# Kernel tuning notes

Hardware: AMD Instinct MI355X
Metric: run time of the kernel (lower is better)

## Reference

```python
import jax, jax.numpy as jnp
import numpy as np
from jax import lax

H = 1028  # hidden_size


def _lstm_layer(x, w_ih, w_hh, b_ih, b_hh):
    # x: [B, T, in], w_ih: [4H, in], w_hh: [4H, H] (PyTorch gate order i,f,g,o)
    B, T, _ = x.shape
    h_dim = w_hh.shape[1]
    # Precompute input contribution for all timesteps (memory-bound GEMM)
    xg = jnp.einsum('bti,gi->btg', x, w_ih) + b_ih + b_hh  # [B, T, 4H]

    def step(carry, xt):
        h, c = carry
        g = xt + h @ w_hh.T  # [B, 4H]
        i, f, gg, o = jnp.split(g, 4, axis=-1)
        i = jax.nn.sigmoid(i)
        f = jax.nn.sigmoid(f)
        gg = jnp.tanh(gg)
        o = jax.nn.sigmoid(o)
        c = f * c + i * gg
        h = o * jnp.tanh(c)
        return (h, c), h

    h0 = jnp.zeros((B, h_dim), x.dtype)
    c0 = jnp.zeros((B, h_dim), x.dtype)
    _, hs = lax.scan(step, (h0, c0), jnp.swapaxes(xg, 0, 1))  # [T, B, H]
    return jnp.swapaxes(hs, 0, 1)  # [B, T, H]


def setup_inputs() -> dict:
    key = jax.random.key(0)
    ks = jax.random.split(key, 12)
    s = 1.0 / np.sqrt(H)  # torch LSTM/Linear init scale

    def u(k, shape):
        return jax.random.uniform(k, shape, jnp.float32, -s, s)

    x = jax.random.normal(ks[0], (1, 16384, 1), dtype=jnp.float32)
    return {
        'x': x,
        'w_ih0': u(ks[1], (4 * H, 1)),
        'w_hh0': u(ks[2], (4 * H, H)),
        'b_ih0': u(ks[3], (4 * H,)),
        'b_hh0': u(ks[4], (4 * H,)),
        'w_ih1': u(ks[5], (4 * H, H)),
        'w_hh1': u(ks[6], (4 * H, H)),
        'b_ih1': u(ks[7], (4 * H,)),
        'b_hh1': u(ks[8], (4 * H,)),
        'lin_w': u(ks[9], (1, H)),
        'lin_b': u(ks[10], (1,)),
    }


def reference(x, w_ih0, w_hh0, b_ih0, b_hh0, w_ih1, w_hh1, b_ih1, b_hh1, lin_w, lin_b):
    h1 = _lstm_layer(x, w_ih0, w_hh0, b_ih0, b_hh0)   # [B, T, H]
    h2 = _lstm_layer(h1, w_ih1, w_hh1, b_ih1, b_hh1)  # [B, T, H]
    return h2 @ lin_w.T + lin_b                        # [B, T, 1]
```

## Files before the change

### kernel.cpp

```cpp
#include <hip/hip_runtime.h>
#include <math.h>

#define HH    1028
#define TT    16384
#define UP    1056
#define HSU   1056
#define HS    1056
#define NWG0  66
#define NWG1  132
#define NWGT  (NWG0 + NWG1)
#define R0    1024
#define R0M   (R0 - 1)
#define R1M   15

typedef unsigned long long u64;

__device__ __forceinline__ u64 ld_u64(const u64* p) {
    return __hip_atomic_load(p, __ATOMIC_RELAXED, __HIP_MEMORY_SCOPE_AGENT);
}
__device__ __forceinline__ void st_u64(u64* p, u64 v) {
    __hip_atomic_store(p, v, __ATOMIC_RELAXED, __HIP_MEMORY_SCOPE_AGENT);
}
__device__ __forceinline__ unsigned ld_u32(const unsigned* p) {
    return __hip_atomic_load(p, __ATOMIC_RELAXED, __HIP_MEMORY_SCOPE_AGENT);
}
__device__ __forceinline__ void st_u32(unsigned* p, unsigned v) {
    __hip_atomic_store(p, v, __ATOMIC_RELAXED, __HIP_MEMORY_SCOPE_AGENT);
}
__device__ __forceinline__ float sigmf(float x) { return 1.0f / (1.0f + expf(-x)); }
__device__ __forceinline__ u64 pack(unsigned tag, float v) {
    return ((u64)tag << 32) | (u64)__float_as_uint(v);
}

__device__ __forceinline__ void stage132(const u64* __restrict__ src, float* __restrict__ lds,
                                         int base, int lane, unsigned want, long long& budget) {
    const int i0 = base + lane, i1 = base + 64 + lane, i2 = base + 128 + lane;
    bool d0 = false, d1 = false, d2 = (lane >= 4);
    int spin = 2;
    for (;;) {
        if (!d0) { u64 v = ld_u64(src + i0);
                   if ((unsigned)(v >> 32) == want) { lds[i0] = __uint_as_float((unsigned)v); d0 = true; } }
        if (!d1) { u64 v = ld_u64(src + i1);
                   if ((unsigned)(v >> 32) == want) { lds[i1] = __uint_as_float((unsigned)v); d1 = true; } }
        if (!d2) { u64 v = ld_u64(src + i2);
                   if ((unsigned)(v >> 32) == want) { lds[i2] = __uint_as_float((unsigned)v); d2 = true; } }
        if (__all(d0 & d1 & d2)) break;
        if (--budget < 0) break;
        if (spin > 0) { --spin; continue; }
        __builtin_amdgcn_s_sleep(1);
    }
}

__device__ __forceinline__ void stage264(const u64* __restrict__ src, float* __restrict__ lds,
                                         int base, int lane, unsigned want, long long& budget) {
    const int i0 = base + lane, i1 = i0 + 64, i2 = i0 + 128, i3 = i0 + 192, i4 = i0 + 256;
    bool d0 = false, d1 = false, d2 = false, d3 = false, d4 = (lane >= 8);
    int spin = 2;
    for (;;) {
        if (!d0) { u64 v = ld_u64(src + i0);
                   if ((unsigned)(v >> 32) == want) { lds[i0] = __uint_as_float((unsigned)v); d0 = true; } }
        if (!d1) { u64 v = ld_u64(src + i1);
                   if ((unsigned)(v >> 32) == want) { lds[i1] = __uint_as_float((unsigned)v); d1 = true; } }
        if (!d2) { u64 v = ld_u64(src + i2);
                   if ((unsigned)(v >> 32) == want) { lds[i2] = __uint_as_float((unsigned)v); d2 = true; } }
        if (!d3) { u64 v = ld_u64(src + i3);
                   if ((unsigned)(v >> 32) == want) { lds[i3] = __uint_as_float((unsigned)v); d3 = true; } }
        if (!d4) { u64 v = ld_u64(src + i4);
                   if ((unsigned)(v >> 32) == want) { lds[i4] = __uint_as_float((unsigned)v); d4 = true; } }
        if (__all(d0 & d1 & d2 & d3 & d4)) break;
        if (--budget < 0) break;
        if (spin > 0) { --spin; continue; }
        __builtin_amdgcn_s_sleep(1);
    }
}

__global__ __launch_bounds__(1024, 4) void wn_fused(
    const float* __restrict__ x,
    const float* __restrict__ w_ih0, const float* __restrict__ w_hh0,
    const float* __restrict__ b_ih0, const float* __restrict__ b_hh0,
    const float* __restrict__ w_ih1, const float* __restrict__ w_hh1,
    const float* __restrict__ b_ih1, const float* __restrict__ b_hh1,
    u64* __restrict__ ring0,
    u64* __restrict__ ring1,
    float* __restrict__ h2hist,
    unsigned* __restrict__ l1prog)
{
    __shared__ float smem[4 * UP + 128];
    const int tid  = threadIdx.x;
    const int lane = tid & 63;
    const int w    = tid >> 6;

    for (int i = tid; i < 4 * UP + 128; i += 1024) smem[i] = 0.0f;

    if (blockIdx.x < NWG0) {
        float* hbuf = smem;
        float* gbuf = smem + 2 * UP;
        const int wg   = blockIdx.x;
        const int row  = tid >> 4;
        const int k0   = tid & 15;
        const int gate = row >> 4;
        const int du   = row & 15;
        const int u    = wg * 16 + du;
        const bool real = (u < HH);
        const int wr   = gate * HH + (real ? u : 0);

        float wv[16][4], wt0 = 0.f, wt1 = 0.f;
#pragma unroll
        for (int m = 0; m < 16; ++m) {
            const int j = k0 * 4 + m * 64;
#pragma unroll
            for (int q = 0; q < 4; ++q)
                wv[m][q] = (real && j + q < HH) ? w_hh0[(size_t)wr * HH + j + q] : 0.0f;
        }
        {   const int j = 1024 + k0 * 2;
            wt0 = (real && j     < HH) ? w_hh0[(size_t)wr * HH + j]     : 0.0f;
            wt1 = (real && j + 1 < HH) ? w_hh0[(size_t)wr * HH + j + 1] : 0.0f; }
#pragma unroll
        for (int m = 0; m < 16; ++m)
#pragma unroll
            for (int q = 0; q < 4; ++q) asm volatile("" : "+v"(wv[m][q]));
        asm volatile("" : "+v"(wt0), "+v"(wt1));

        const float wx = real ? w_ih0[wr] : 0.0f;
        const float bs = real ? (b_ih0[wr] + b_hh0[wr]) : 0.0f;
        __syncthreads();

        long long budget = 20000000LL;
        float c_reg = 0.0f;
        for (int t = 0; t < TT; ++t) {
            if (t > 0) {
                if (w == 0) {
                    const float* gl = gbuf + ((t - 1) & 1) * 64;
                    if (lane < 16) {
                        const float gi = gl[lane], gf = gl[16 + lane];
                        const float gg = gl[32 + lane], go = gl[48 + lane];
                        const float iv = sigmf(gi), fv = sigmf(gf), gv = tanhf(gg), ov = sigmf(go);
                        c_reg = fv * c_reg + iv * gv;
                        float hv = ov * tanhf(c_reg);
                        if (wg * 16 + lane >= HH) hv = 0.0f;
                        st_u64(ring0 + (size_t)((t - 1) & R0M) * HSU + wg * 16 + lane,
                               pack((unsigned)t, hv));
                    }
                } else if (w >= 4 && w < 12) {
                    stage132(ring0 + (size_t)((t - 1) & R0M) * HSU, hbuf + (t & 1) * UP,
                             (w - 4) * 132, lane, (unsigned)t, budget);
                } else if (w == 1 && lane == 0 && (t & 255) == 0) {
                    for (;;) {
                        unsigned p = ld_u32(l1prog);
                        if ((int)t - (int)p < R0 - 256) break;
                        if (--budget < 0) break;
                        __builtin_amdgcn_s_sleep(32);
                    }
                }
            }
            __syncthreads();
            const float* hb = hbuf + (t & 1) * UP;
            float acc = 0.0f;
#pragma unroll
            for (int m = 0; m < 16; ++m) {
                const float4 hv = *(const float4*)&hb[k0 * 4 + m * 64];
                acc = fmaf(wv[m][0], hv.x, acc);
                acc = fmaf(wv[m][1], hv.y, acc);
                acc = fmaf(wv[m][2], hv.z, acc);
                acc = fmaf(wv[m][3], hv.w, acc);
            }
            {   const float2 hv = *(const float2*)&hb[1024 + k0 * 2];
                acc = fmaf(wt0, hv.x, acc);
                acc = fmaf(wt1, hv.y, acc); }
#pragma unroll
            for (int off = 1; off < 16; off <<= 1) acc += __shfl_xor(acc, off);
            if (k0 == 0) gbuf[(t & 1) * 64 + row] = acc + x[t] * wx + bs;
            __syncthreads();
        }
        if (w == 0 && lane < 16) {
            const float* gl = gbuf + ((TT - 1) & 1) * 64;
            const float gi = gl[lane], gf = gl[16 + lane];
            const float gg = gl[32 + lane], go = gl[48 + lane];
            const float iv = sigmf(gi), fv = sigmf(gf), gv = tanhf(gg), ov = sigmf(go);
            c_reg = fv * c_reg + iv * gv;
            float hv = ov * tanhf(c_reg);
            if (wg * 16 + lane >= HH) hv = 0.0f;
            st_u64(ring0 + (size_t)((TT - 1) & R0M) * HSU + wg * 16 + lane,
                   pack((unsigned)TT, hv));
        }
    } else {
        float* abuf = smem;
        float* bbuf = smem + 2 * UP;
        float* gbuf = smem + 4 * UP;
        const int wg   = blockIdx.x - NWG0;
        const int row  = tid >> 5;
        const int k0   = tid & 31;
        const int gate = row >> 3;
        const int du   = row & 7;
        const int u    = wg * 8 + du;
        const bool real = (u < HH);
        const int wr   = gate * HH + (real ? u : 0);

        float wiv[8][4], whv[8][4], wit = 0.f, wht = 0.f;
#pragma unroll
        for (int m = 0; m < 8; ++m) {
            const int j = k0 * 4 + m * 128;
#pragma unroll
            for (int q = 0; q < 4; ++q) {
                const bool inb = real && (j + q < HH);
                wiv[m][q] = inb ? w_ih1[(size_t)wr * HH + j + q] : 0.0f;
                whv[m][q] = inb ? w_hh1[(size_t)wr * HH + j + q] : 0.0f;
            }
        }
        {   const int j = 1024 + k0;
            wit = (real && j < HH) ? w_ih1[(size_t)wr * HH + j] : 0.0f;
            wht = (real && j < HH) ? w_hh1[(size_t)wr * HH + j] : 0.0f; }
#pragma unroll
        for (int m = 0; m < 8; ++m)
#pragma unroll
            for (int q = 0; q < 4; ++q) {
                asm volatile("" : "+v"(wiv[m][q]));
                asm volatile("" : "+v"(whv[m][q]));
            }
        asm volatile("" : "+v"(wit), "+v"(wht));
        const float bs = real ? (b_ih1[wr] + b_hh1[wr]) : 0.0f;
        __syncthreads();

        long long budget = 20000000LL;
        float c_reg = 0.0f;
        for (int t = 0; t < TT; ++t) {
            if (w == 0) {
                if (t > 0) {
                    const float* gl = gbuf + ((t - 1) & 1) * 32;
                    if (lane < 8) {
                        const float gi = gl[lane], gf = gl[8 + lane];
                        const float gg = gl[16 + lane], go = gl[24 + lane];
                        const float iv = sigmf(gi), fv = sigmf(gf), gv = tanhf(gg), ov = sigmf(go);
                        c_reg = fv * c_reg + iv * gv;
                        float hv = ov * tanhf(c_reg);
                        if (wg * 8 + lane >= HH) hv = 0.0f;
                        st_u64(ring1 + (size_t)((t - 1) & R1M) * HSU + wg * 8 + lane,
                               pack((unsigned)t, hv));
                        h2hist[(size_t)(t - 1) * HS + wg * 8 + lane] = hv;
                    }
                }
            } else if (w >= 4 && w < 12) {
                if (t > 0)
                    stage132(ring1 + (size_t)((t - 1) & R1M) * HSU, bbuf + (t & 1) * UP,
                             (w - 4) * 132, lane, (unsigned)t, budget);
            } else if (w >= 12) {
                stage264(ring0 + (size_t)(t & R0M) * HSU, abuf + (t & 1) * UP,
                         (w - 12) * 264, lane, (unsigned)(t + 1), budget);
            }
            __syncthreads();
            const float* ab = abuf + (t & 1) * UP;
            const float* bb = bbuf + (t & 1) * UP;
            float acc = 0.0f;
#pragma unroll
            for (int m = 0; m < 8; ++m) {
                const float4 ha = *(const float4*)&ab[k0 * 4 + m * 128];
                const float4 hb2 = *(const float4*)&bb[k0 * 4 + m * 128];
                acc = fmaf(wiv[m][0], ha.x, acc);
                acc = fmaf(wiv[m][1], ha.y, acc);
                acc = fmaf(wiv[m][2], ha.z, acc);
                acc = fmaf(wiv[m][3], ha.w, acc);
                acc = fmaf(whv[m][0], hb2.x, acc);
                acc = fmaf(whv[m][1], hb2.y, acc);
                acc = fmaf(whv[m][2], hb2.z, acc);
                acc = fmaf(whv[m][3], hb2.w, acc);
            }
            acc = fmaf(wit, ab[1024 + k0], acc);
            acc = fmaf(wht, bb[1024 + k0], acc);
#pragma unroll
            for (int off = 1; off < 32; off <<= 1) acc += __shfl_xor(acc, off);
            if (k0 == 0) gbuf[(t & 1) * 32 + row] = acc + bs;
            __syncthreads();
            if (w == 1 && lane == 0 && wg == 0 && (t & 255) == 255)
                st_u32(l1prog, (unsigned)(t + 1));
        }
        if (w == 0 && lane < 8) {
            const float* gl = gbuf + ((TT - 1) & 1) * 32;
            const float gi = gl[lane], gf = gl[8 + lane];
            const float gg = gl[16 + lane], go = gl[24 + lane];
            const float iv = sigmf(gi), fv = sigmf(gf), gv = tanhf(gg), ov = sigmf(go);
            c_reg = fv * c_reg + iv * gv;
            float hv = ov * tanhf(c_reg);
            if (wg * 8 + lane >= HH) hv = 0.0f;
            h2hist[(size_t)(TT - 1) * HS + wg * 8 + lane] = hv;
        }
    }
}

__global__ __launch_bounds__(256) void wn_proj(
    const float* __restrict__ h2,
    const float* __restrict__ lin_w,
    const float* __restrict__ lin_b,
    float* __restrict__ out)
{
    const int lane = threadIdx.x & 63;
    const int wv   = threadIdx.x >> 6;
    const int t    = blockIdx.x * 4 + wv;
    const float* hp = h2 + (size_t)t * HS;
    float acc = 0.0f;
#pragma unroll
    for (int m = 0; m < 4; ++m) {
        const int j = lane * 4 + m * 256;
        const float4 h4 = *(const float4*)(hp + j);
        const float4 w4 = *(const float4*)(lin_w + j);
        acc += h4.x * w4.x + h4.y * w4.y + h4.z * w4.z + h4.w * w4.w;
    }
    if (lane == 0) {
#pragma unroll
        for (int j = 1024; j < HH; ++j) acc += hp[j] * lin_w[j];
    }
#pragma unroll
    for (int off = 1; off < 64; off <<= 1) acc += __shfl_xor(acc, off);
    if (lane == 0) out[t] = acc + lin_b[0];
}

extern "C" void kernel_launch(void* const* d_in, const int* in_sizes, int n_in,
                              void* d_out, int out_size, void* d_ws, size_t ws_size,
                              hipStream_t stream) {
    const float* x     = (const float*)d_in[0];
    const float* w_ih0 = (const float*)d_in[1];
    const float* w_hh0 = (const float*)d_in[2];
    const float* b_ih0 = (const float*)d_in[3];
    const float* b_hh0 = (const float*)d_in[4];
    const float* w_ih1 = (const float*)d_in[5];
    const float* w_hh1 = (const float*)d_in[6];
    const float* b_ih1 = (const float*)d_in[7];
    const float* b_hh1 = (const float*)d_in[8];
    const float* lin_w = (const float*)d_in[9];
    const float* lin_b = (const float*)d_in[10];
    float* out = (float*)d_out;

    char* ws = (char*)d_ws;
    const size_t R0B = (size_t)R0 * HSU * 8;
    const size_t R1B = (size_t)16 * HSU * 8;
    const size_t H2B = (size_t)TT * HS * 4;
    u64* ring0 = (u64*)(ws);
    u64* ring1 = (u64*)(ws + R0B);
    float* h2hist = (float*)(ws + R0B + R1B);
    unsigned* l1prog = (unsigned*)(ws + R0B + R1B + H2B);

    wn_fused<<<NWGT, 1024, 0, stream>>>(x, w_ih0, w_hh0, b_ih0, b_hh0,
                                        w_ih1, w_hh1, b_ih1, b_hh1,
                                        ring0, ring1, h2hist, l1prog);
    wn_proj<<<TT / 4, 256, 0, stream>>>(h2hist, lin_w, lin_b, out);
}
```

Baseline: 43.81 ms.

## Remap waves so each owns one hidden unit and drop the second barrier per step

Work is reassigned so each wavefront computes all four gate dot products for one hidden unit (layer 0) or a gate pair (layer 1). The gate nonlinearities and the cell update now happen in registers via shuffles, which removes the LDS gate buffer and the second __syncthreads per timestep. Every wave now also takes part in staging the ring data. In layer 1, the g/o waves hand their results to the i/f waves through LDS slots tagged with the step number and read by spin-waiting. The aim is to shorten the serial per-step critical path. The cost is extra spin polling, and the intra-workgroup LDS handshake is a correctness risk because it relies on relaxed atomics with no barrier.

```diff
diff --git a/kernel.cpp b/kernel.cpp
--- a/kernel.cpp
+++ b/kernel.cpp
@@ -27,9 +27,32 @@
 __device__ __forceinline__ void st_u32(unsigned* p, unsigned v) {
     __hip_atomic_store(p, v, __ATOMIC_RELAXED, __HIP_MEMORY_SCOPE_AGENT);
 }
+__device__ __forceinline__ u64 ld_lds_u64(const u64* p) {
+    return __hip_atomic_load(p, __ATOMIC_RELAXED, __HIP_MEMORY_SCOPE_WORKGROUP);
+}
+__device__ __forceinline__ void st_lds_u64(u64* p, u64 v) {
+    __hip_atomic_store(p, v, __ATOMIC_RELAXED, __HIP_MEMORY_SCOPE_WORKGROUP);
+}
 __device__ __forceinline__ float sigmf(float x) { return 1.0f / (1.0f + expf(-x)); }
 __device__ __forceinline__ u64 pack(unsigned tag, float v) {
     return ((u64)tag << 32) | (u64)__float_as_uint(v);
+}
+
+__device__ __forceinline__ void stage66(const u64* __restrict__ src, float* __restrict__ lds,
+                                        int base, int lane, unsigned want, long long& budget) {
+    const int i0 = base + lane, i1 = base + 64 + lane;
+    bool d0 = false, d1 = (lane >= 2);
+    int spin = 2;
+    for (;;) {
+        if (!d0) { u64 v = ld_u64(src + i0);
+                   if ((unsigned)(v >> 32) == want) { lds[i0] = __uint_as_float((unsigned)v); d0 = true; } }
+        if (!d1) { u64 v = ld_u64(src + i1);
+                   if ((unsigned)(v >> 32) == want) { lds[i1] = __uint_as_float((unsigned)v); d1 = true; } }
+        if (__all(d0 & d1)) break;
+        if (--budget < 0) break;
+        if (spin > 0) { --spin; continue; }
+        __builtin_amdgcn_s_sleep(1);
+    }
 }
 
 __device__ __forceinline__ void stage132(const u64* __restrict__ src, float* __restrict__ lds,
@@ -51,29 +74,6 @@
     }
 }
 
-__device__ __forceinline__ void stage264(const u64* __restrict__ src, float* __restrict__ lds,
-                                         int base, int lane, unsigned want, long long& budget) {
-    const int i0 = base + lane, i1 = i0 + 64, i2 = i0 + 128, i3 = i0 + 192, i4 = i0 + 256;
-    bool d0 = false, d1 = false, d2 = false, d3 = false, d4 = (lane >= 8);
-    int spin = 2;
-    for (;;) {
-        if (!d0) { u64 v = ld_u64(src + i0);
-                   if ((unsigned)(v >> 32) == want) { lds[i0] = __uint_as_float((unsigned)v); d0 = true; } }
-        if (!d1) { u64 v = ld_u64(src + i1);
-                   if ((unsigned)(v >> 32) == want) { lds[i1] = __uint_as_float((unsigned)v); d1 = true; } }
-        if (!d2) { u64 v = ld_u64(src + i2);
-                   if ((unsigned)(v >> 32) == want) { lds[i2] = __uint_as_float((unsigned)v); d2 = true; } }
-        if (!d3) { u64 v = ld_u64(src + i3);
-                   if ((unsigned)(v >> 32) == want) { lds[i3] = __uint_as_float((unsigned)v); d3 = true; } }
-        if (!d4) { u64 v = ld_u64(src + i4);
-                   if ((unsigned)(v >> 32) == want) { lds[i4] = __uint_as_float((unsigned)v); d4 = true; } }
-        if (__all(d0 & d1 & d2 & d3 & d4)) break;
-        if (--budget < 0) break;
-        if (spin > 0) { --spin; continue; }
-        __builtin_amdgcn_s_sleep(1);
-    }
-}
-
 __global__ __launch_bounds__(1024, 4) void wn_fused(
     const float* __restrict__ x,
     const float* __restrict__ w_ih0, const float* __restrict__ w_hh0,
@@ -85,34 +85,31 @@
     float* __restrict__ h2hist,
     unsigned* __restrict__ l1prog)
 {
-    __shared__ float smem[4 * UP + 128];
+    __shared__ float smem[4 * UP + 32];
     const int tid  = threadIdx.x;
     const int lane = tid & 63;
     const int w    = tid >> 6;
 
-    for (int i = tid; i < 4 * UP + 128; i += 1024) smem[i] = 0.0f;
+    for (int i = tid; i < 4 * UP + 32; i += 1024) smem[i] = 0.0f;
 
     if (blockIdx.x < NWG0) {
         float* hbuf = smem;
-        float* gbuf = smem + 2 * UP;
         const int wg   = blockIdx.x;
-        const int row  = tid >> 4;
-        const int k0   = tid & 15;
-        const int gate = row >> 4;
-        const int du   = row & 15;
-        const int u    = wg * 16 + du;
+        const int u    = wg * 16 + w;
+        const int gate = lane >> 4;
+        const int kc   = lane & 15;
         const bool real = (u < HH);
         const int wr   = gate * HH + (real ? u : 0);
 
         float wv[16][4], wt0 = 0.f, wt1 = 0.f;
 #pragma unroll
         for (int m = 0; m < 16; ++m) {
-            const int j = k0 * 4 + m * 64;
+            const int j = kc * 4 + m * 64;
 #pragma unroll
             for (int q = 0; q < 4; ++q)
                 wv[m][q] = (real && j + q < HH) ? w_hh0[(size_t)wr * HH + j + q] : 0.0f;
         }
-        {   const int j = 1024 + k0 * 2;
+        {   const int j = 1024 + kc * 2;
             wt0 = (real && j     < HH) ? w_hh0[(size_t)wr * HH + j]     : 0.0f;
             wt1 = (real && j + 1 < HH) ? w_hh0[(size_t)wr * HH + j + 1] : 0.0f; }
 #pragma unroll
@@ -128,78 +125,62 @@
         long long budget = 20000000LL;
         float c_reg = 0.0f;
         for (int t = 0; t < TT; ++t) {
-            if (t > 0) {
-                if (w == 0) {
-                    const float* gl = gbuf + ((t - 1) & 1) * 64;
-                    if (lane < 16) {
-                        const float gi = gl[lane], gf = gl[16 + lane];
-                        const float gg = gl[32 + lane], go = gl[48 + lane];
-                        const float iv = sigmf(gi), fv = sigmf(gf), gv = tanhf(gg), ov = sigmf(go);
-                        c_reg = fv * c_reg + iv * gv;
-                        float hv = ov * tanhf(c_reg);
-                        if (wg * 16 + lane >= HH) hv = 0.0f;
-                        st_u64(ring0 + (size_t)((t - 1) & R0M) * HSU + wg * 16 + lane,
-                               pack((unsigned)t, hv));
-                    }
-                } else if (w >= 4 && w < 12) {
-                    stage132(ring0 + (size_t)((t - 1) & R0M) * HSU, hbuf + (t & 1) * UP,
-                             (w - 4) * 132, lane, (unsigned)t, budget);
-                } else if (w == 1 && lane == 0 && (t & 255) == 0) {
-                    for (;;) {
-                        unsigned p = ld_u32(l1prog);
-                        if ((int)t - (int)p < R0 - 256) break;
-                        if (--budget < 0) break;
-                        __builtin_amdgcn_s_sleep(32);
-                    }
+            const float xt = x[t];
+            if (w == 0 && lane == 63 && t > 0 && (t & 255) == 0) {
+                for (;;) {
+                    unsigned p = ld_u32(l1prog);
+                    if ((int)t - (int)p < R0 - 256) break;
+                    if (--budget < 0) break;
+                    __builtin_amdgcn_s_sleep(32);
                 }
             }
+            if (t > 0)
+                stage66(ring0 + (size_t)((t - 1) & R0M) * HSU, hbuf + (t & 1) * UP,
+                        w * 66, lane, (unsigned)t, budget);
             __syncthreads();
             const float* hb = hbuf + (t & 1) * UP;
             float acc = 0.0f;
 #pragma unroll
             for (int m = 0; m < 16; ++m) {
-                const float4 hv = *(const float4*)&hb[k0 * 4 + m * 64];
-                acc = fmaf(wv[m][0], hv.x, acc);
-                acc = fmaf(wv[m][1], hv.y, acc);
-                acc = fmaf(wv[m][2], hv.z, acc);
-                acc = fmaf(wv[m][3], hv.w, acc);
-            }
-            {   const float2 hv = *(const float2*)&hb[1024 + k0 * 2];
-                acc = fmaf(wt0, hv.x, acc);
-                acc = fmaf(wt1, hv.y, acc); }
+                const float4 hv4 = *(const float4*)&hb[kc * 4 + m * 64];
+                acc = fmaf(wv[m][0], hv4.x, acc);
+                acc = fmaf(wv[m][1], hv4.y, acc);
+                acc = fmaf(wv[m][2], hv4.z, acc);
+                acc = fmaf(wv[m][3], hv4.w, acc);
+            }
+            {   const float2 hv2 = *(const float2*)&hb[1024 + kc * 2];
+                acc = fmaf(wt0, hv2.x, acc);
+                acc = fmaf(wt1, hv2.y, acc); }
 #pragma unroll
             for (int off = 1; off < 16; off <<= 1) acc += __shfl_xor(acc, off);
-            if (k0 == 0) gbuf[(t & 1) * 64 + row] = acc + x[t] * wx + bs;
-            __syncthreads();
-        }
-        if (w == 0 && lane < 16) {
-            const float* gl = gbuf + ((TT - 1) & 1) * 64;
-            const float gi = gl[lane], gf = gl[16 + lane];
-            const float gg = gl[32 + lane], go = gl[48 + lane];
-            const float iv = sigmf(gi), fv = sigmf(gf), gv = tanhf(gg), ov = sigmf(go);
+            acc = fmaf(xt, wx, acc) + bs;
+            const float si = __shfl(acc, 0),  sf = __shfl(acc, 16);
+            const float sg = __shfl(acc, 32), so = __shfl(acc, 48);
+            const float iv = sigmf(si), fv = sigmf(sf), gv = tanhf(sg), ov = sigmf(so);
             c_reg = fv * c_reg + iv * gv;
             float hv = ov * tanhf(c_reg);
-            if (wg * 16 + lane >= HH) hv = 0.0f;
-            st_u64(ring0 + (size_t)((TT - 1) & R0M) * HSU + wg * 16 + lane,
-                   pack((unsigned)TT, hv));
+            if (!real) hv = 0.0f;
+            if (lane == 0)
+                st_u64(ring0 + (size_t)(t & R0M) * HSU + u, pack((unsigned)(t + 1), hv));
         }
     } else {
         float* abuf = smem;
         float* bbuf = smem + 2 * UP;
-        float* gbuf = smem + 4 * UP;
+        u64*   pair = (u64*)(smem + 4 * UP);
         const int wg   = blockIdx.x - NWG0;
-        const int row  = tid >> 5;
-        const int k0   = tid & 31;
-        const int gate = row >> 3;
-        const int du   = row & 7;
+        const bool isIF = (w < 8);
+        const int du   = isIF ? w : (w - 8);
         const int u    = wg * 8 + du;
+        const int g2   = lane >> 5;
+        const int gate = (isIF ? 0 : 2) + g2;
+        const int kc   = lane & 31;
         const bool real = (u < HH);
         const int wr   = gate * HH + (real ? u : 0);
 
         float wiv[8][4], whv[8][4], wit = 0.f, wht = 0.f;
 #pragma unroll
         for (int m = 0; m < 8; ++m) {
-            const int j = k0 * 4 + m * 128;
+            const int j = kc * 4 + m * 128;
 #pragma unroll
             for (int q = 0; q < 4; ++q) {
                 const bool inb = real && (j + q < HH);
@@ -207,7 +188,7 @@
                 whv[m][q] = inb ? w_hh1[(size_t)wr * HH + j + q] : 0.0f;
             }
         }
-        {   const int j = 1024 + k0;
+        {   const int j = 1024 + kc;
             wit = (real && j < HH) ? w_ih1[(size_t)wr * HH + j] : 0.0f;
             wht = (real && j < HH) ? w_hh1[(size_t)wr * HH + j] : 0.0f; }
 #pragma unroll
@@ -224,28 +205,13 @@
         long long budget = 20000000LL;
         float c_reg = 0.0f;
         for (int t = 0; t < TT; ++t) {
-            if (w == 0) {
-                if (t > 0) {
-                    const float* gl = gbuf + ((t - 1) & 1) * 32;
-                    if (lane < 8) {
-                        const float gi = gl[lane], gf = gl[8 + lane];
-                        const float gg = gl[16 + lane], go = gl[24 + lane];
-                        const float iv = sigmf(gi), fv = sigmf(gf), gv = tanhf(gg), ov = sigmf(go);
-                        c_reg = fv * c_reg + iv * gv;
-                        float hv = ov * tanhf(c_reg);
-                        if (wg * 8 + lane >= HH) hv = 0.0f;
-                        st_u64(ring1 + (size_t)((t - 1) & R1M) * HSU + wg * 8 + lane,
-                               pack((unsigned)t, hv));
-                        h2hist[(size_t)(t - 1) * HS + wg * 8 + lane] = hv;
-                    }
-                }
-            } else if (w >= 4 && w < 12) {
+            if (isIF) {
                 if (t > 0)
                     stage132(ring1 + (size_t)((t - 1) & R1M) * HSU, bbuf + (t & 1) * UP,
-                             (w - 4) * 132, lane, (unsigned)t, budget);
-            } else if (w >= 12) {
-                stage264(ring0 + (size_t)(t & R0M) * HSU, abuf + (t & 1) * UP,
-                         (w - 12) * 264, lane, (unsigned)(t + 1), budget);
+                             du * 132, lane, (unsigned)t, budget);
+            } else {
+                stage132(ring0 + (size_t)(t & R0M) * HSU, abuf + (t & 1) * UP,
+                         du * 132, lane, (unsigned)(t + 1), budget);
             }
             __syncthreads();
             const float* ab = abuf + (t & 1) * UP;
@@ -253,8 +219,8 @@
             float acc = 0.0f;
 #pragma unroll
             for (int m = 0; m < 8; ++m) {
-                const float4 ha = *(const float4*)&ab[k0 * 4 + m * 128];
-                const float4 hb2 = *(const float4*)&bb[k0 * 4 + m * 128];
+                const float4 ha  = *(const float4*)&ab[kc * 4 + m * 128];
+                const float4 hb2 = *(const float4*)&bb[kc * 4 + m * 128];
                 acc = fmaf(wiv[m][0], ha.x, acc);
                 acc = fmaf(wiv[m][1], ha.y, acc);
                 acc = fmaf(wiv[m][2], ha.z, acc);
@@ -264,24 +230,42 @@
                 acc = fmaf(whv[m][2], hb2.z, acc);
                 acc = fmaf(whv[m][3], hb2.w, acc);
             }
-            acc = fmaf(wit, ab[1024 + k0], acc);
-            acc = fmaf(wht, bb[1024 + k0], acc);
+            acc = fmaf(wit, ab[1024 + kc], acc);
+            acc = fmaf(wht, bb[1024 + kc], acc);
 #pragma unroll
             for (int off = 1; off < 32; off <<= 1) acc += __shfl_xor(acc, off);
-            if (k0 == 0) gbuf[(t & 1) * 32 + row] = acc + bs;
-            __syncthreads();
-            if (w == 1 && lane == 0 && wg == 0 && (t & 255) == 255)
-                st_u32(l1prog, (unsigned)(t + 1));
-        }
-        if (w == 0 && lane < 8) {
-            const float* gl = gbuf + ((TT - 1) & 1) * 32;
-            const float gi = gl[lane], gf = gl[8 + lane];
-            const float gg = gl[16 + lane], go = gl[24 + lane];
-            const float iv = sigmf(gi), fv = sigmf(gf), gv = tanhf(gg), ov = sigmf(go);
-            c_reg = fv * c_reg + iv * gv;
-            float hv = ov * tanhf(c_reg);
-            if (wg * 8 + lane >= HH) hv = 0.0f;
-            h2hist[(size_t)(TT - 1) * HS + wg * 8 + lane] = hv;
+            acc += bs;
+            if (!isIF) {
+                const float sg_ = __shfl(acc, 0), so_ = __shfl(acc, 32);
+                if (lane == 0) {
+                    st_lds_u64(&pair[du * 2 + 0], pack((unsigned)(t + 1), sg_));
+                    st_lds_u64(&pair[du * 2 + 1], pack((unsigned)(t + 1), so_));
+                }
+            } else {
+                const float si = __shfl(acc, 0), sf = __shfl(acc, 32);
+                float sg = 0.f, so = 0.f;
+                const unsigned want = (unsigned)(t + 1);
+                for (;;) {
+                    u64 a = ld_lds_u64(&pair[du * 2 + 0]);
+                    u64 b = ld_lds_u64(&pair[du * 2 + 1]);
+                    if ((unsigned)(a >> 32) == want && (unsigned)(b >> 32) == want) {
+                        sg = __uint_as_float((unsigned)a);
+                        so = __uint_as_float((unsigned)b);
+                        break;
+                    }
+                    if (--budget < 0) break;
+                }
+                const float iv = sigmf(si), fv = sigmf(sf), gv = tanhf(sg), ov = sigmf(so);
+                c_reg = fv * c_reg + iv * gv;
+                float hv = ov * tanhf(c_reg);
+                if (!real) hv = 0.0f;
+                if (lane == 0) {
+                    st_u64(ring1 + (size_t)(t & R1M) * HSU + u, pack((unsigned)(t + 1), hv));
+                    h2hist[(size_t)t * HS + u] = hv;
+                }
+                if (wg == 0 && w == 1 && lane == 0 && (t & 255) == 255)
+                    st_u32(l1prog, (unsigned)(t + 1));
+            }
         }
     }
 }
```

After: 85.94 ms. +96.2%, slower.
